# Performance work log

Hardware: AMD Instinct MI355X
Metric: run time of the kernel (lower is better)

Reference implementation:

```python
import jax, jax.numpy as jnp
from jax import lax
import numpy as np

IMG = 500
FM = 31
RATIOS = [1.0, 2.0, 0.5]
SCALES = [128, 256, 512]
PRE_NMS = 6000
POST_NMS = 1500  # train_nms_topn (test=False)
IOU_THR = 0.7
VARIANCES = np.array([0.1, 0.1, 0.2, 0.2], np.float32)
BATCH = 16


def _gen_anchors():
    # bbox_utils.generate_anchors: normalized [y1,x1,y2,x2], grid of 31x31 centers,
    # 9 base shapes from (scale, ratio), clipped to [0,1].
    ctr = (np.arange(FM, dtype=np.float32) + 0.5) / FM
    cy, cx = np.meshgrid(ctr, ctr, indexing='ij')          # [FM,FM]
    base = []
    for s in SCALES:
        for r in RATIOS:
            w = s * np.sqrt(r) / IMG
            h = s / np.sqrt(r) / IMG
            base.append([h, w])
    base = np.array(base, np.float32)                       # [9,2]
    h, w = base[:, 0], base[:, 1]
    cy = cy[..., None]; cx = cx[..., None]                  # [FM,FM,1]
    anc = np.stack([cy - h / 2, cx - w / 2, cy + h / 2, cx + w / 2], axis=-1)
    return np.clip(anc.reshape(-1, 4), 0.0, 1.0).astype(np.float32)  # [8649,4]


def setup_inputs() -> dict:
    key = jax.random.key(0)
    k1, k2 = jax.random.split(key)
    return {
        'rpn_bbox_deltas': jax.random.normal(k1, (BATCH, FM, FM, 36), jnp.float32),
        'rpn_probs': jax.random.uniform(k2, (BATCH, FM, FM, 9), jnp.float32),
        'anchors': jnp.asarray(_gen_anchors()),
    }


def _nms_keep(boxes, scores):
    # Greedy NMS over score-descending-sorted boxes; returns keep mask [N].
    N = boxes.shape[0]
    y1, x1, y2, x2 = boxes[:, 0], boxes[:, 1], boxes[:, 2], boxes[:, 3]
    area = (y2 - y1) * (x2 - x1)

    def body(i, state):
        supp, keep, cnt = state
        valid = jnp.logical_and(jnp.logical_not(supp[i]), cnt < POST_NMS)
        keep = keep.at[i].set(valid)
        cnt = cnt + valid.astype(jnp.int32)
        ih = jnp.maximum(jnp.minimum(y2[i], y2) - jnp.maximum(y1[i], y1), 0.0)
        iw = jnp.maximum(jnp.minimum(x2[i], x2) - jnp.maximum(x1[i], x1), 0.0)
        inter = ih * iw
        iou = inter / (area[i] + area - inter + 1e-8)
        supp = jnp.where(valid, jnp.logical_or(supp, iou > IOU_THR), supp)
        return supp, keep, cnt

    supp0 = jnp.zeros((N,), bool)
    keep0 = jnp.zeros((N,), bool)
    _, keep, _ = lax.fori_loop(0, N, body, (supp0, keep0, jnp.int32(0)))
    return keep


def reference(rpn_bbox_deltas, rpn_probs, anchors):
    B = rpn_bbox_deltas.shape[0]
    N = anchors.shape[0]
    deltas = rpn_bbox_deltas.reshape(B, N, 4) * jnp.asarray(VARIANCES)  # [B,N,4]
    probs = rpn_probs.reshape(B, N)                                     # [B,N]

    # decode anchor deltas -> boxes
    anc_h = anchors[:, 2] - anchors[:, 0]
    anc_w = anchors[:, 3] - anchors[:, 1]
    ctr_y = anchors[:, 0] + 0.5 * anc_h
    ctr_x = anchors[:, 1] + 0.5 * anc_w
    bh = jnp.exp(deltas[..., 2]) * anc_h
    bw = jnp.exp(deltas[..., 3]) * anc_w
    bcy = deltas[..., 0] * anc_h + ctr_y
    bcx = deltas[..., 1] * anc_w + ctr_x
    y1 = bcy - 0.5 * bh
    x1 = bcx - 0.5 * bw
    boxes = jnp.stack([y1, x1, y1 + bh, x1 + bw], axis=-1)              # [B,N,4]

    # pre-NMS top-k by objectness (sorted descending)
    top_scores, top_idx = lax.top_k(probs, PRE_NMS)                     # [B,PRE_NMS]
    top_boxes = jnp.take_along_axis(boxes, top_idx[..., None], axis=1)  # [B,PRE_NMS,4]

    # greedy NMS (selection is non-differentiable, compute on stopped values)
    keep = jax.vmap(_nms_keep)(lax.stop_gradient(top_boxes),
                               lax.stop_gradient(top_scores))           # [B,PRE_NMS] bool

    # compact kept entries to the front, zero-pad to POST_NMS (combined NMS semantics)
    rank = jnp.cumsum(keep, axis=1) - 1
    slot = jnp.where(keep, rank, POST_NMS)  # dropped entries go to overflow slot

    def _scatter(sl, bx, sc, k):
        ob = jnp.zeros((POST_NMS + 1, 4), bx.dtype).at[sl].set(jnp.where(k[:, None], bx, 0.0))
        os = jnp.zeros((POST_NMS + 1,), sc.dtype).at[sl].set(jnp.where(k, sc, 0.0))
        return ob[:POST_NMS], os[:POST_NMS]

    roi_bboxes, roi_scores = jax.vmap(_scatter)(slot, top_boxes, top_scores, keep)
    roi_bboxes = jnp.clip(roi_bboxes, 0.0, 1.0)  # clip_boxes=True in combined NMS
    return roi_bboxes, roi_scores
```

## Files before the change

### kernel.cpp

```cpp
#include <hip/hip_runtime.h>
#include <hip/hip_bf16.h>

#define BATCH   16
#define N_ANC   8649
#define SORT_N  16384
#define PRE     6000
#define POST    1500
#define ROWW    188
#define MROWS   6016
#define NGRP    188
#define TI      256
#define TJ      256

__global__ __launch_bounds__(256) void k_decode(
    const float* __restrict__ deltas, const float* __restrict__ probs,
    const float* __restrict__ anchors, float4* __restrict__ boxes,
    unsigned long long* __restrict__ keys)
{
    int t = blockIdx.x * 256 + threadIdx.x;
    if (t >= BATCH * SORT_N) return;
    int b = t / SORT_N;
    int n = t - b * SORT_N;
    if (n >= N_ANC) { keys[t] = ~0ULL; return; }

    float s = probs[(size_t)b * N_ANC + n];
    unsigned int bits = __float_as_uint(s);
    unsigned int u = bits ^ ((bits & 0x80000000u) ? 0xFFFFFFFFu : 0x80000000u);
    keys[(size_t)b * SORT_N + n] = ((unsigned long long)(~u) << 32) | (unsigned int)n;

    float4 a = ((const float4*)anchors)[n];
    float4 d = ((const float4*)deltas)[(size_t)b * N_ANC + n];
    float dy = d.x * 0.1f, dx = d.y * 0.1f, dh = d.z * 0.2f, dw = d.w * 0.2f;
    float ah = a.z - a.x, aw = a.w - a.y;
    float cy = a.x + 0.5f * ah, cx = a.y + 0.5f * aw;
    float bh = expf(dh) * ah, bw = expf(dw) * aw;
    float bcy = dy * ah + cy, bcx = dx * aw + cx;
    float y1 = bcy - 0.5f * bh, x1 = bcx - 0.5f * bw;
    boxes[(size_t)b * N_ANC + n] = make_float4(y1, x1, y1 + bh, x1 + bw);
}

__global__ __launch_bounds__(1024) void k_sort(unsigned long long* __restrict__ keys)
{
    __shared__ unsigned long long sb[8192];
    int b = blockIdx.x;
    unsigned long long* kb = keys + (size_t)b * SORT_N;

    for (int c = 0; c < 2; c++) {
        unsigned long long* g = kb + c * 8192;
        for (int t = threadIdx.x; t < 8192; t += 1024) sb[t] = g[t];
        __syncthreads();
        for (int k = 2; k <= 8192; k <<= 1) {
            for (int j = k >> 1; j >= 1; j >>= 1) {
                for (int p = threadIdx.x; p < 4096; p += 1024) {
                    int i  = ((p & ~(j - 1)) << 1) | (p & (j - 1));
                    int gi = (c << 13) | i;
                    bool asc = ((gi & k) == 0);
                    unsigned long long a = sb[i], b2 = sb[i | j];
                    bool sw = asc ? (a > b2) : (a < b2);
                    if (sw) { sb[i] = b2; sb[i | j] = a; }
                }
                __syncthreads();
            }
        }
        for (int t = threadIdx.x; t < 8192; t += 1024) g[t] = sb[t];
        __syncthreads();
    }

    for (int p = threadIdx.x; p < 8192; p += 1024) {
        unsigned long long a = kb[p], b2 = kb[p + 8192];
        if (a > b2) { kb[p] = b2; kb[p + 8192] = a; }
    }
    __syncthreads();

    for (int t = threadIdx.x; t < 8192; t += 1024) sb[t] = kb[t];
    __syncthreads();
    for (int j = 4096; j >= 1; j >>= 1) {
        for (int p = threadIdx.x; p < 4096; p += 1024) {
            int i = ((p & ~(j - 1)) << 1) | (p & (j - 1));
            unsigned long long a = sb[i], b2 = sb[i | j];
            if (a > b2) { sb[i] = b2; sb[i | j] = a; }
        }
        __syncthreads();
    }
    for (int t = threadIdx.x; t < 6016; t += 1024) kb[t] = sb[t];
}

__global__ __launch_bounds__(256) void k_gather(
    const unsigned long long* __restrict__ keys, const float4* __restrict__ boxes,
    const float* __restrict__ probs,
    float4* __restrict__ sboxes, float* __restrict__ sscores)
{
    int t = blockIdx.x * 256 + threadIdx.x;
    if (t >= BATCH * PRE) return;
    int b = t / PRE;
    int r = t - b * PRE;
    unsigned long long k = keys[(size_t)b * SORT_N + r];
    int idx = (int)(k & 0xFFFFFFFFu);
    sboxes[(size_t)b * PRE + r]  = boxes[(size_t)b * N_ANC + idx];
    sscores[(size_t)b * PRE + r] = probs[(size_t)b * N_ANC + idx];
}

__global__ __launch_bounds__(256) void k_iou(
    const float4* __restrict__ sboxes, unsigned int* __restrict__ mask,
    unsigned int* __restrict__ diag)
{
    int it = blockIdx.x;
    int jt = blockIdx.y;
    int b  = blockIdx.z;
    if (jt < it) return;

    __shared__ float4 jb[TJ];
    __shared__ float  ja[TJ];
    int t = threadIdx.x;
    int j = jt * TJ + t;
    float4 bj = (j < PRE) ? sboxes[(size_t)b * PRE + j]
                          : make_float4(-2e6f, -2e6f, -1.5e6f, -1.5e6f);
    jb[t] = bj;
    ja[t] = (bj.z - bj.x) * (bj.w - bj.y);
    __syncthreads();

    int i = it * TI + t;
    if (i >= PRE) return;
    float4 bi = sboxes[(size_t)b * PRE + i];
    float areai = (bi.z - bi.x) * (bi.w - bi.y);

    unsigned int w[8];
    if (jt > it) {
        for (int wq = 0; wq < 8; wq++) {
            unsigned int bits = 0u;
            #pragma unroll
            for (int jj = 0; jj < 32; jj++) {
                int lj = wq * 32 + jj;
                float4 bx = jb[lj];
                float ih = fmaxf(fminf(bi.z, bx.z) - fmaxf(bi.x, bx.x), 0.0f);
                float iw = fmaxf(fminf(bi.w, bx.w) - fmaxf(bi.y, bx.y), 0.0f);
                float inter = ih * iw;
                float iou = inter / (areai + ja[lj] - inter + 1e-8f);
                if (iou > 0.7f) bits |= (1u << jj);
            }
            w[wq] = bits;
        }
    } else {
        unsigned int dw = 0u;
        for (int wq = 0; wq < 8; wq++) {
            int jbase = jt * TJ + wq * 32;
            unsigned int bits = 0u;
            if (jbase + 31 > i) {
                #pragma unroll
                for (int jj = 0; jj < 32; jj++) {
                    int lj = wq * 32 + jj;
                    float4 bx = jb[lj];
                    float ih = fmaxf(fminf(bi.z, bx.z) - fmaxf(bi.x, bx.x), 0.0f);
                    float iw = fmaxf(fminf(bi.w, bx.w) - fmaxf(bi.y, bx.y), 0.0f);
                    float inter = ih * iw;
                    float iou = inter / (areai + ja[lj] - inter + 1e-8f);
                    if (iou > 0.7f && (jbase + jj) > i) bits |= (1u << jj);
                }
            }
            w[wq] = bits;
            if (wq == (t >> 5)) dw = bits;
        }
        diag[(size_t)b * MROWS + it * 256 + t] = dw;
    }

    unsigned int* row = mask + ((size_t)b * MROWS + i) * ROWW + jt * 8;
    ((uint4*)row)[0] = make_uint4(w[0], w[1], w[2], w[3]);
    if (jt < 23) ((uint4*)row)[1] = make_uint4(w[4], w[5], w[6], w[7]);
}

__global__ __launch_bounds__(64, 1) void k_scan(
    const unsigned int* __restrict__ mask, const unsigned int* __restrict__ diag,
    int* __restrict__ out_idx, int* __restrict__ out_cnt)
{
    int b = blockIdx.x;
    int lane = threadIdx.x;
    const unsigned int* mb = mask + (size_t)b * MROWS * ROWW;
    const unsigned int* db = diag + (size_t)b * MROWS;
    bool lact = (lane < 47);
    unsigned int lbit  = 1u << (lane & 31);
    unsigned int below = lbit - 1u;

    uint4 st = make_uint4(0, 0, 0, 0);
    int cnt = 0;
    int* oi = out_idx + b * POST;

    for (int g = 0; g < NGRP; g++) {
        const uint4* dt = (const uint4*)(db + g * 32);
        uint4 t0 = dt[0], t1 = dt[1], t2 = dt[2], t3 = dt[3];
        uint4 t4 = dt[4], t5 = dt[5], t6 = dt[6], t7 = dt[7];

        bool need = lact && (4 * lane + 3 >= g);
        const unsigned int* gp = mb + (size_t)g * 32 * ROWW + 4 * lane;
        uint4 r[32];
        #pragma unroll
        for (int k = 0; k < 32; k++)
            r[k] = need ? *(const uint4*)(gp + (size_t)k * ROWW)
                        : make_uint4(0, 0, 0, 0);

        unsigned int cword = (g & 2) ? ((g & 1) ? st.w : st.z)
                                     : ((g & 1) ? st.y : st.x);
        unsigned int swv = __shfl(cword, g >> 2);

        unsigned int tri[32];
        tri[0]=t0.x;  tri[1]=t0.y;  tri[2]=t0.z;  tri[3]=t0.w;
        tri[4]=t1.x;  tri[5]=t1.y;  tri[6]=t1.z;  tri[7]=t1.w;
        tri[8]=t2.x;  tri[9]=t2.y;  tri[10]=t2.z; tri[11]=t2.w;
        tri[12]=t3.x; tri[13]=t3.y; tri[14]=t3.z; tri[15]=t3.w;
        tri[16]=t4.x; tri[17]=t4.y; tri[18]=t4.z; tri[19]=t4.w;
        tri[20]=t5.x; tri[21]=t5.y; tri[22]=t5.z; tri[23]=t5.w;
        tri[24]=t6.x; tri[25]=t6.y; tri[26]=t6.z; tri[27]=t6.w;
        tri[28]=t7.x; tri[29]=t7.y; tri[30]=t7.z; tri[31]=t7.w;

        unsigned int valid = (g == NGRP - 1) ? 0xFFFFu : 0xFFFFFFFFu;
        unsigned int alive = ~swv & valid;
        unsigned int keepm = 0;
        #pragma unroll
        for (int k = 0; k < 32; k++) {
            unsigned int bit = (alive >> k) & 1u;
            keepm |= bit << k;
            alive &= ~((0u - bit) & tri[k]);
        }

        int need_n = POST - cnt;
        int rank = __popc(keepm & below);
        bool keep_me = (lane < 32) && (keepm & lbit) && (rank < need_n);
        unsigned long long bal = __ballot(keep_me);
        unsigned int keepm2 = (unsigned int)bal;
        if (keep_me) oi[cnt + rank] = g * 32 + lane;

        #pragma unroll
        for (int k = 0; k < 32; k++) {
            unsigned int m = 0u - ((keepm2 >> k) & 1u);
            st.x |= r[k].x & m; st.y |= r[k].y & m;
            st.z |= r[k].z & m; st.w |= r[k].w & m;
        }

        cnt += __popc(keepm2);
        if (cnt >= POST) break;
    }
    if (lane == 0) out_cnt[b] = cnt;
}

__global__ __launch_bounds__(256) void k_out(
    const float4* __restrict__ sboxes, const float* __restrict__ sscores,
    const int* __restrict__ out_idx, const int* __restrict__ out_cnt,
    float* __restrict__ out)
{
    int t = blockIdx.x * 256 + threadIdx.x;
    if (t >= BATCH * POST) return;
    int b = t / POST;
    int r = t - b * POST;
    float4 v = make_float4(0, 0, 0, 0);
    float sc = 0.f;
    if (r < out_cnt[b]) {
        int i = out_idx[b * POST + r];
        float4 bx = sboxes[(size_t)b * PRE + i];
        v.x = fminf(fmaxf(bx.x, 0.f), 1.f);
        v.y = fminf(fmaxf(bx.y, 0.f), 1.f);
        v.z = fminf(fmaxf(bx.z, 0.f), 1.f);
        v.w = fminf(fmaxf(bx.w, 0.f), 1.f);
        sc = sscores[(size_t)b * PRE + i];
    }
    ((float4*)out)[t] = v;
    out[(size_t)BATCH * POST * 4 + t] = sc;
}

extern "C" void kernel_launch(void* const* d_in, const int* in_sizes, int n_in,
                              void* d_out, int out_size, void* d_ws, size_t ws_size,
                              hipStream_t stream)
{
    const float* deltas  = (const float*)d_in[0];
    const float* probs   = (const float*)d_in[1];
    const float* anchors = (const float*)d_in[2];
    float* out = (float*)d_out;

    char* ws = (char*)d_ws;
    size_t off = 0;
    auto alloc = [&](size_t bytes) {
        size_t o = off;
        off = (off + bytes + 255) & ~(size_t)255;
        return o;
    };
    float4* boxes            = (float4*)(ws + alloc((size_t)BATCH * N_ANC * 16));
    unsigned long long* keys = (unsigned long long*)(ws + alloc((size_t)BATCH * SORT_N * 8));
    float4* sboxes           = (float4*)(ws + alloc((size_t)BATCH * PRE * 16));
    float* sscores           = (float*)(ws + alloc((size_t)BATCH * PRE * 4));
    unsigned int* mask       = (unsigned int*)(ws + alloc((size_t)BATCH * MROWS * ROWW * 4));
    unsigned int* diag       = (unsigned int*)(ws + alloc((size_t)BATCH * MROWS * 4));
    int* oidx                = (int*)(ws + alloc((size_t)BATCH * POST * 4));
    int* ocnt                = (int*)(ws + alloc((size_t)BATCH * 4));

    k_decode<<<(BATCH * SORT_N + 255) / 256, 256, 0, stream>>>(deltas, probs, anchors, boxes, keys);
    k_sort<<<BATCH, 1024, 0, stream>>>(keys);
    k_gather<<<(BATCH * PRE + 255) / 256, 256, 0, stream>>>(keys, boxes, probs, sboxes, sscores);
    k_iou<<<dim3(24, 24, BATCH), 256, 0, stream>>>(sboxes, mask, diag);
    k_scan<<<BATCH, 64, 0, stream>>>(mask, diag, oidx, ocnt);
    k_out<<<(BATCH * POST + 255) / 256, 256, 0, stream>>>(sboxes, sscores, oidx, ocnt, out);
}
```

Baseline: 710.8 us.

## Split IoU mask and scan into two phases to skip unneeded tiles

```diff
diff --git a/kernel.cpp b/kernel.cpp
--- a/kernel.cpp
+++ b/kernel.cpp
@@ -9,6 +9,7 @@
 #define ROWW    188
 #define MROWS   6016
 #define NGRP    188
+#define GLIM    64
 #define TI      256
 #define TJ      256
 
@@ -100,14 +101,16 @@
     sscores[(size_t)b * PRE + r] = probs[(size_t)b * N_ANC + idx];
 }
 
+template<int IT0, bool CHK>
 __global__ __launch_bounds__(256) void k_iou(
     const float4* __restrict__ sboxes, unsigned int* __restrict__ mask,
-    unsigned int* __restrict__ diag)
-{
-    int it = blockIdx.x;
+    unsigned int* __restrict__ diag, const int* __restrict__ done)
+{
+    int it = IT0 + blockIdx.x;
     int jt = blockIdx.y;
     int b  = blockIdx.z;
     if (jt < it) return;
+    if (CHK && done[b]) return;
 
     __shared__ float4 jb[TJ];
     __shared__ float  ja[TJ];
@@ -168,9 +171,10 @@
     if (jt < 23) ((uint4*)row)[1] = make_uint4(w[4], w[5], w[6], w[7]);
 }
 
-__global__ __launch_bounds__(64, 1) void k_scan(
+__global__ __launch_bounds__(64, 1) void k_scan_a(
     const unsigned int* __restrict__ mask, const unsigned int* __restrict__ diag,
-    int* __restrict__ out_idx, int* __restrict__ out_cnt)
+    int* __restrict__ out_idx, int* __restrict__ out_cnt,
+    uint4* __restrict__ stbuf, int* __restrict__ done)
 {
     int b = blockIdx.x;
     int lane = threadIdx.x;
@@ -184,7 +188,7 @@
     int cnt = 0;
     int* oi = out_idx + b * POST;
 
-    for (int g = 0; g < NGRP; g++) {
+    for (int g = 0; g < GLIM; g++) {
         const uint4* dt = (const uint4*)(db + g * 32);
         uint4 t0 = dt[0], t1 = dt[1], t2 = dt[2], t3 = dt[3];
         uint4 t4 = dt[4], t5 = dt[5], t6 = dt[6], t7 = dt[7];
@@ -211,8 +215,7 @@
         tri[24]=t6.x; tri[25]=t6.y; tri[26]=t6.z; tri[27]=t6.w;
         tri[28]=t7.x; tri[29]=t7.y; tri[30]=t7.z; tri[31]=t7.w;
 
-        unsigned int valid = (g == NGRP - 1) ? 0xFFFFu : 0xFFFFFFFFu;
-        unsigned int alive = ~swv & valid;
+        unsigned int alive = ~swv;
         unsigned int keepm = 0;
         #pragma unroll
         for (int k = 0; k < 32; k++) {
@@ -234,7 +237,81 @@
             st.x |= r[k].x & m; st.y |= r[k].y & m;
             st.z |= r[k].z & m; st.w |= r[k].w & m;
         }
-
+        cnt += __popc(keepm2);
+    }
+
+    if (lact) stbuf[b * 47 + lane] = st;
+    if (lane == 0) { out_cnt[b] = cnt; done[b] = (cnt >= POST) ? 1 : 0; }
+}
+
+__global__ __launch_bounds__(64, 1) void k_scan_b(
+    const unsigned int* __restrict__ mask, const unsigned int* __restrict__ diag,
+    int* __restrict__ out_idx, int* __restrict__ out_cnt,
+    const uint4* __restrict__ stbuf, const int* __restrict__ done)
+{
+    int b = blockIdx.x;
+    if (done[b]) return;
+    int lane = threadIdx.x;
+    const unsigned int* mb = mask + (size_t)b * MROWS * ROWW;
+    const unsigned int* db = diag + (size_t)b * MROWS;
+    bool lact = (lane < 47);
+    unsigned int lbit  = 1u << (lane & 31);
+    unsigned int below = lbit - 1u;
+
+    uint4 st = lact ? stbuf[b * 47 + lane] : make_uint4(0, 0, 0, 0);
+    int cnt = out_cnt[b];
+    int* oi = out_idx + b * POST;
+
+    for (int g = GLIM; g < NGRP; g++) {
+        const uint4* dt = (const uint4*)(db + g * 32);
+        uint4 t0 = dt[0], t1 = dt[1], t2 = dt[2], t3 = dt[3];
+        uint4 t4 = dt[4], t5 = dt[5], t6 = dt[6], t7 = dt[7];
+
+        bool need = lact && (4 * lane + 3 >= g);
+        const unsigned int* gp = mb + (size_t)g * 32 * ROWW + 4 * lane;
+        uint4 r[32];
+        #pragma unroll
+        for (int k = 0; k < 32; k++)
+            r[k] = need ? *(const uint4*)(gp + (size_t)k * ROWW)
+                        : make_uint4(0, 0, 0, 0);
+
+        unsigned int cword = (g & 2) ? ((g & 1) ? st.w : st.z)
+                                     : ((g & 1) ? st.y : st.x);
+        unsigned int swv = __shfl(cword, g >> 2);
+
+        unsigned int tri[32];
+        tri[0]=t0.x;  tri[1]=t0.y;  tri[2]=t0.z;  tri[3]=t0.w;
+        tri[4]=t1.x;  tri[5]=t1.y;  tri[6]=t1.z;  tri[7]=t1.w;
+        tri[8]=t2.x;  tri[9]=t2.y;  tri[10]=t2.z; tri[11]=t2.w;
+        tri[12]=t3.x; tri[13]=t3.y; tri[14]=t3.z; tri[15]=t3.w;
+        tri[16]=t4.x; tri[17]=t4.y; tri[18]=t4.z; tri[19]=t4.w;
+        tri[20]=t5.x; tri[21]=t5.y; tri[22]=t5.z; tri[23]=t5.w;
+        tri[24]=t6.x; tri[25]=t6.y; tri[26]=t6.z; tri[27]=t6.w;
+        tri[28]=t7.x; tri[29]=t7.y; tri[30]=t7.z; tri[31]=t7.w;
+
+        unsigned int valid = (g == NGRP - 1) ? 0xFFFFu : 0xFFFFFFFFu;
+        unsigned int alive = ~swv & valid;
+        unsigned int keepm = 0;
+        #pragma unroll
+        for (int k = 0; k < 32; k++) {
+            unsigned int bit = (alive >> k) & 1u;
+            keepm |= bit << k;
+            alive &= ~((0u - bit) & tri[k]);
+        }
+
+        int need_n = POST - cnt;
+        int rank = __popc(keepm & below);
+        bool keep_me = (lane < 32) && (keepm & lbit) && (rank < need_n);
+        unsigned long long bal = __ballot(keep_me);
+        unsigned int keepm2 = (unsigned int)bal;
+        if (keep_me) oi[cnt + rank] = g * 32 + lane;
+
+        #pragma unroll
+        for (int k = 0; k < 32; k++) {
+            unsigned int m = 0u - ((keepm2 >> k) & 1u);
+            st.x |= r[k].x & m; st.y |= r[k].y & m;
+            st.z |= r[k].z & m; st.w |= r[k].w & m;
+        }
         cnt += __popc(keepm2);
         if (cnt >= POST) break;
     }
@@ -289,11 +366,15 @@
     unsigned int* diag       = (unsigned int*)(ws + alloc((size_t)BATCH * MROWS * 4));
     int* oidx                = (int*)(ws + alloc((size_t)BATCH * POST * 4));
     int* ocnt                = (int*)(ws + alloc((size_t)BATCH * 4));
+    uint4* stbuf             = (uint4*)(ws + alloc((size_t)BATCH * 47 * 16));
+    int* done                = (int*)(ws + alloc((size_t)BATCH * 4));
 
     k_decode<<<(BATCH * SORT_N + 255) / 256, 256, 0, stream>>>(deltas, probs, anchors, boxes, keys);
     k_sort<<<BATCH, 1024, 0, stream>>>(keys);
     k_gather<<<(BATCH * PRE + 255) / 256, 256, 0, stream>>>(keys, boxes, probs, sboxes, sscores);
-    k_iou<<<dim3(24, 24, BATCH), 256, 0, stream>>>(sboxes, mask, diag);
-    k_scan<<<BATCH, 64, 0, stream>>>(mask, diag, oidx, ocnt);
+    k_iou<0, false><<<dim3(8, 24, BATCH), 256, 0, stream>>>(sboxes, mask, diag, done);
+    k_scan_a<<<BATCH, 64, 0, stream>>>(mask, diag, oidx, ocnt, stbuf, done);
+    k_iou<8, true><<<dim3(16, 24, BATCH), 256, 0, stream>>>(sboxes, mask, diag, done);
+    k_scan_b<<<BATCH, 64, 0, stream>>>(mask, diag, oidx, ocnt, stbuf, done);
     k_out<<<(BATCH * POST + 255) / 256, 256, 0, stream>>>(sboxes, sscores, oidx, ocnt, out);
 }
```

After: 779.2 us. 9.6% more time.

## Split sort across blocks, widen IoU tiles, double-buffer NMS scan loads

Applied to the files above, without the earlier changes.

```diff
diff --git a/kernel.cpp b/kernel.cpp
--- a/kernel.cpp
+++ b/kernel.cpp
@@ -6,11 +6,9 @@
 #define SORT_N  16384
 #define PRE     6000
 #define POST    1500
-#define ROWW    188
+#define RWORDS  192
 #define MROWS   6016
 #define NGRP    188
-#define TI      256
-#define TJ      256
 
 __global__ __launch_bounds__(256) void k_decode(
     const float* __restrict__ deltas, const float* __restrict__ probs,
@@ -39,32 +37,36 @@
     boxes[(size_t)b * N_ANC + n] = make_float4(y1, x1, y1 + bh, x1 + bw);
 }
 
-__global__ __launch_bounds__(1024) void k_sort(unsigned long long* __restrict__ keys)
+__global__ __launch_bounds__(1024) void k_sort_chunk(unsigned long long* __restrict__ keys)
+{
+    __shared__ unsigned long long sb[8192];
+    int b = blockIdx.x >> 1;
+    int c = blockIdx.x & 1;
+    unsigned long long* g = keys + (size_t)b * SORT_N + c * 8192;
+
+    for (int t = threadIdx.x; t < 8192; t += 1024) sb[t] = g[t];
+    __syncthreads();
+    for (int k = 2; k <= 8192; k <<= 1) {
+        for (int j = k >> 1; j >= 1; j >>= 1) {
+            for (int p = threadIdx.x; p < 4096; p += 1024) {
+                int i  = ((p & ~(j - 1)) << 1) | (p & (j - 1));
+                int gi = (c << 13) | i;
+                bool asc = ((gi & k) == 0);
+                unsigned long long a = sb[i], b2 = sb[i | j];
+                bool sw = asc ? (a > b2) : (a < b2);
+                if (sw) { sb[i] = b2; sb[i | j] = a; }
+            }
+            __syncthreads();
+        }
+    }
+    for (int t = threadIdx.x; t < 8192; t += 1024) g[t] = sb[t];
+}
+
+__global__ __launch_bounds__(1024) void k_sort_merge(unsigned long long* __restrict__ keys)
 {
     __shared__ unsigned long long sb[8192];
     int b = blockIdx.x;
     unsigned long long* kb = keys + (size_t)b * SORT_N;
-
-    for (int c = 0; c < 2; c++) {
-        unsigned long long* g = kb + c * 8192;
-        for (int t = threadIdx.x; t < 8192; t += 1024) sb[t] = g[t];
-        __syncthreads();
-        for (int k = 2; k <= 8192; k <<= 1) {
-            for (int j = k >> 1; j >= 1; j >>= 1) {
-                for (int p = threadIdx.x; p < 4096; p += 1024) {
-                    int i  = ((p & ~(j - 1)) << 1) | (p & (j - 1));
-                    int gi = (c << 13) | i;
-                    bool asc = ((gi & k) == 0);
-                    unsigned long long a = sb[i], b2 = sb[i | j];
-                    bool sw = asc ? (a > b2) : (a < b2);
-                    if (sw) { sb[i] = b2; sb[i | j] = a; }
-                }
-                __syncthreads();
-            }
-        }
-        for (int t = threadIdx.x; t < 8192; t += 1024) g[t] = sb[t];
-        __syncthreads();
-    }
 
     for (int p = threadIdx.x; p < 8192; p += 1024) {
         unsigned long long a = kb[p], b2 = kb[p + 8192];
@@ -107,66 +109,104 @@
     int it = blockIdx.x;
     int jt = blockIdx.y;
     int b  = blockIdx.z;
-    if (jt < it) return;
-
-    __shared__ float4 jb[TJ];
-    __shared__ float  ja[TJ];
+    int ibase = it * 1024;
+    int jbase0 = jt * 256;
+    if (jbase0 + 255 <= ibase) return;
+
+    __shared__ float4 jb[256];
+    __shared__ float  ja[256];
     int t = threadIdx.x;
-    int j = jt * TJ + t;
+    int j = jbase0 + t;
     float4 bj = (j < PRE) ? sboxes[(size_t)b * PRE + j]
                           : make_float4(-2e6f, -2e6f, -1.5e6f, -1.5e6f);
     jb[t] = bj;
     ja[t] = (bj.z - bj.x) * (bj.w - bj.y);
     __syncthreads();
 
-    int i = it * TI + t;
-    if (i >= PRE) return;
-    float4 bi = sboxes[(size_t)b * PRE + i];
-    float areai = (bi.z - bi.x) * (bi.w - bi.y);
-
-    unsigned int w[8];
-    if (jt > it) {
-        for (int wq = 0; wq < 8; wq++) {
-            unsigned int bits = 0u;
+    float4 bi[4];
+    float  ai[4];
+    int    ir[4];
+    #pragma unroll
+    for (int r = 0; r < 4; r++) {
+        ir[r] = ibase + t + 256 * r;
+        bi[r] = (ir[r] < PRE) ? sboxes[(size_t)b * PRE + ir[r]]
+                              : make_float4(0.f, 0.f, 0.f, 0.f);
+        ai[r] = (bi[r].z - bi[r].x) * (bi[r].w - bi[r].y);
+    }
+
+    unsigned int w[4][8];
+    for (int wq = 0; wq < 8; wq++) {
+        int jbase = jbase0 + wq * 32;
+        unsigned int bits0 = 0, bits1 = 0, bits2 = 0, bits3 = 0;
+        #pragma unroll
+        for (int jj = 0; jj < 32; jj++) {
+            int lj = wq * 32 + jj;
+            float4 bx = jb[lj];
+            float  aj = ja[lj];
+            int    jg = jbase + jj;
             #pragma unroll
-            for (int jj = 0; jj < 32; jj++) {
-                int lj = wq * 32 + jj;
-                float4 bx = jb[lj];
-                float ih = fmaxf(fminf(bi.z, bx.z) - fmaxf(bi.x, bx.x), 0.0f);
-                float iw = fmaxf(fminf(bi.w, bx.w) - fmaxf(bi.y, bx.y), 0.0f);
+            for (int r = 0; r < 4; r++) {
+                float ih = fmaxf(fminf(bi[r].z, bx.z) - fmaxf(bi[r].x, bx.x), 0.0f);
+                float iw = fmaxf(fminf(bi[r].w, bx.w) - fmaxf(bi[r].y, bx.y), 0.0f);
                 float inter = ih * iw;
-                float iou = inter / (areai + ja[lj] - inter + 1e-8f);
-                if (iou > 0.7f) bits |= (1u << jj);
+                float iou = inter / (ai[r] + aj - inter + 1e-8f);
+                bool set = (iou > 0.7f) && (jg > ir[r]);
+                unsigned int bit = set ? (1u << jj) : 0u;
+                if (r == 0) bits0 |= bit;
+                else if (r == 1) bits1 |= bit;
+                else if (r == 2) bits2 |= bit;
+                else bits3 |= bit;
             }
-            w[wq] = bits;
-        }
-    } else {
-        unsigned int dw = 0u;
-        for (int wq = 0; wq < 8; wq++) {
-            int jbase = jt * TJ + wq * 32;
-            unsigned int bits = 0u;
-            if (jbase + 31 > i) {
-                #pragma unroll
-                for (int jj = 0; jj < 32; jj++) {
-                    int lj = wq * 32 + jj;
-                    float4 bx = jb[lj];
-                    float ih = fmaxf(fminf(bi.z, bx.z) - fmaxf(bi.x, bx.x), 0.0f);
-                    float iw = fmaxf(fminf(bi.w, bx.w) - fmaxf(bi.y, bx.y), 0.0f);
-                    float inter = ih * iw;
-                    float iou = inter / (areai + ja[lj] - inter + 1e-8f);
-                    if (iou > 0.7f && (jbase + jj) > i) bits |= (1u << jj);
-                }
-            }
-            w[wq] = bits;
-            if (wq == (t >> 5)) dw = bits;
-        }
-        diag[(size_t)b * MROWS + it * 256 + t] = dw;
-    }
-
-    unsigned int* row = mask + ((size_t)b * MROWS + i) * ROWW + jt * 8;
-    ((uint4*)row)[0] = make_uint4(w[0], w[1], w[2], w[3]);
-    if (jt < 23) ((uint4*)row)[1] = make_uint4(w[4], w[5], w[6], w[7]);
-}
+        }
+        w[0][wq] = bits0; w[1][wq] = bits1; w[2][wq] = bits2; w[3][wq] = bits3;
+    }
+
+    #pragma unroll
+    for (int r = 0; r < 4; r++) {
+        if (ir[r] < PRE) {
+            unsigned int* row = mask + ((size_t)b * MROWS + ir[r]) * RWORDS + jt * 8;
+            ((uint4*)row)[0] = make_uint4(w[r][0], w[r][1], w[r][2], w[r][3]);
+            ((uint4*)row)[1] = make_uint4(w[r][4], w[r][5], w[r][6], w[r][7]);
+            if ((ir[r] >> 8) == jt)
+                diag[(size_t)b * MROWS + ir[r]] = w[r][(ir[r] >> 5) & 7];
+        }
+    }
+}
+
+#define PROCESS_GROUP(G, R, T)                                                   \
+    do {                                                                         \
+        unsigned int cw_ = ((G) & 2) ? (((G) & 1) ? st.w : st.z)                 \
+                                     : (((G) & 1) ? st.y : st.x);                \
+        unsigned int swv_ = __shfl(cw_, (G) >> 2);                               \
+        unsigned int tri_[32];                                                   \
+        _Pragma("unroll")                                                        \
+        for (int q_ = 0; q_ < 8; q_++) {                                         \
+            tri_[4*q_]   = T[q_].x; tri_[4*q_+1] = T[q_].y;                      \
+            tri_[4*q_+2] = T[q_].z; tri_[4*q_+3] = T[q_].w;                      \
+        }                                                                        \
+        unsigned int valid_ = ((G) == NGRP - 1) ? 0xFFFFu : 0xFFFFFFFFu;         \
+        unsigned int alive_ = ~swv_ & valid_;                                    \
+        unsigned int keepm_ = 0;                                                 \
+        _Pragma("unroll")                                                        \
+        for (int k_ = 0; k_ < 32; k_++) {                                        \
+            unsigned int bit_ = (alive_ >> k_) & 1u;                             \
+            keepm_ |= bit_ << k_;                                                \
+            alive_ &= ~((0u - bit_) & tri_[k_]);                                 \
+        }                                                                        \
+        int need_ = POST - cnt;                                                  \
+        int rank_ = __popc(keepm_ & below);                                      \
+        bool kme_ = (lane < 32) && (keepm_ & lbit) && (rank_ < need_);           \
+        unsigned long long bal_ = __ballot(kme_);                                \
+        unsigned int km2_ = (unsigned int)bal_;                                  \
+        if (kme_) oi[cnt + rank_] = (G) * 32 + lane;                             \
+        _Pragma("unroll")                                                        \
+        for (int k_ = 0; k_ < 32; k_++) {                                        \
+            unsigned int m_ = 0u - ((km2_ >> k_) & 1u);                          \
+            st.x |= R[k_].x & m_; st.y |= R[k_].y & m_;                          \
+            st.z |= R[k_].z & m_; st.w |= R[k_].w & m_;                          \
+        }                                                                        \
+        cnt += __popc(km2_);                                                     \
+    } while (0)
 
 __global__ __launch_bounds__(64, 1) void k_scan(
     const unsigned int* __restrict__ mask, const unsigned int* __restrict__ diag,
@@ -174,9 +214,8 @@
 {
     int b = blockIdx.x;
     int lane = threadIdx.x;
-    const unsigned int* mb = mask + (size_t)b * MROWS * ROWW;
+    const uint4* m4 = (const uint4*)(mask + (size_t)b * MROWS * RWORDS);
     const unsigned int* db = diag + (size_t)b * MROWS;
-    bool lact = (lane < 47);
     unsigned int lbit  = 1u << (lane & 31);
     unsigned int below = lbit - 1u;
 
@@ -184,59 +223,34 @@
     int cnt = 0;
     int* oi = out_idx + b * POST;
 
-    for (int g = 0; g < NGRP; g++) {
-        const uint4* dt = (const uint4*)(db + g * 32);
-        uint4 t0 = dt[0], t1 = dt[1], t2 = dt[2], t3 = dt[3];
-        uint4 t4 = dt[4], t5 = dt[5], t6 = dt[6], t7 = dt[7];
-
-        bool need = lact && (4 * lane + 3 >= g);
-        const unsigned int* gp = mb + (size_t)g * 32 * ROWW + 4 * lane;
-        uint4 r[32];
+    uint4 rA[32], rB[32];
+    uint4 tA[8],  tB[8];
+
+    #pragma unroll
+    for (int k = 0; k < 32; k++) rA[k] = m4[(size_t)k * 48 + lane];
+    #pragma unroll
+    for (int q = 0; q < 8; q++) tA[q] = ((const uint4*)db)[q];
+
+    for (int g = 0; g < NGRP; g += 2) {
         #pragma unroll
         for (int k = 0; k < 32; k++)
-            r[k] = need ? *(const uint4*)(gp + (size_t)k * ROWW)
-                        : make_uint4(0, 0, 0, 0);
-
-        unsigned int cword = (g & 2) ? ((g & 1) ? st.w : st.z)
-                                     : ((g & 1) ? st.y : st.x);
-        unsigned int swv = __shfl(cword, g >> 2);
-
-        unsigned int tri[32];
-        tri[0]=t0.x;  tri[1]=t0.y;  tri[2]=t0.z;  tri[3]=t0.w;
-        tri[4]=t1.x;  tri[5]=t1.y;  tri[6]=t1.z;  tri[7]=t1.w;
-        tri[8]=t2.x;  tri[9]=t2.y;  tri[10]=t2.z; tri[11]=t2.w;
-        tri[12]=t3.x; tri[13]=t3.y; tri[14]=t3.z; tri[15]=t3.w;
-        tri[16]=t4.x; tri[17]=t4.y; tri[18]=t4.z; tri[19]=t4.w;
-        tri[20]=t5.x; tri[21]=t5.y; tri[22]=t5.z; tri[23]=t5.w;
-        tri[24]=t6.x; tri[25]=t6.y; tri[26]=t6.z; tri[27]=t6.w;
-        tri[28]=t7.x; tri[29]=t7.y; tri[30]=t7.z; tri[31]=t7.w;
-
-        unsigned int valid = (g == NGRP - 1) ? 0xFFFFu : 0xFFFFFFFFu;
-        unsigned int alive = ~swv & valid;
-        unsigned int keepm = 0;
+            rB[k] = m4[(size_t)((g + 1) * 32 + k) * 48 + lane];
         #pragma unroll
-        for (int k = 0; k < 32; k++) {
-            unsigned int bit = (alive >> k) & 1u;
-            keepm |= bit << k;
-            alive &= ~((0u - bit) & tri[k]);
-        }
-
-        int need_n = POST - cnt;
-        int rank = __popc(keepm & below);
-        bool keep_me = (lane < 32) && (keepm & lbit) && (rank < need_n);
-        unsigned long long bal = __ballot(keep_me);
-        unsigned int keepm2 = (unsigned int)bal;
-        if (keep_me) oi[cnt + rank] = g * 32 + lane;
-
-        #pragma unroll
-        for (int k = 0; k < 32; k++) {
-            unsigned int m = 0u - ((keepm2 >> k) & 1u);
-            st.x |= r[k].x & m; st.y |= r[k].y & m;
-            st.z |= r[k].z & m; st.w |= r[k].w & m;
-        }
-
-        cnt += __popc(keepm2);
-        if (cnt >= POST) break;
+        for (int q = 0; q < 8; q++)
+            tB[q] = ((const uint4*)(db + (g + 1) * 32))[q];
+
+        PROCESS_GROUP(g, rA, tA);
+
+        if (g + 2 < NGRP) {
+            #pragma unroll
+            for (int k = 0; k < 32; k++)
+                rA[k] = m4[(size_t)((g + 2) * 32 + k) * 48 + lane];
+            #pragma unroll
+            for (int q = 0; q < 8; q++)
+                tA[q] = ((const uint4*)(db + (g + 2) * 32))[q];
+        }
+
+        PROCESS_GROUP(g + 1, rB, tB);
     }
     if (lane == 0) out_cnt[b] = cnt;
 }
@@ -285,15 +299,16 @@
     unsigned long long* keys = (unsigned long long*)(ws + alloc((size_t)BATCH * SORT_N * 8));
     float4* sboxes           = (float4*)(ws + alloc((size_t)BATCH * PRE * 16));
     float* sscores           = (float*)(ws + alloc((size_t)BATCH * PRE * 4));
-    unsigned int* mask       = (unsigned int*)(ws + alloc((size_t)BATCH * MROWS * ROWW * 4));
+    unsigned int* mask       = (unsigned int*)(ws + alloc((size_t)BATCH * MROWS * RWORDS * 4));
     unsigned int* diag       = (unsigned int*)(ws + alloc((size_t)BATCH * MROWS * 4));
     int* oidx                = (int*)(ws + alloc((size_t)BATCH * POST * 4));
     int* ocnt                = (int*)(ws + alloc((size_t)BATCH * 4));
 
     k_decode<<<(BATCH * SORT_N + 255) / 256, 256, 0, stream>>>(deltas, probs, anchors, boxes, keys);
-    k_sort<<<BATCH, 1024, 0, stream>>>(keys);
+    k_sort_chunk<<<BATCH * 2, 1024, 0, stream>>>(keys);
+    k_sort_merge<<<BATCH, 1024, 0, stream>>>(keys);
     k_gather<<<(BATCH * PRE + 255) / 256, 256, 0, stream>>>(keys, boxes, probs, sboxes, sscores);
-    k_iou<<<dim3(24, 24, BATCH), 256, 0, stream>>>(sboxes, mask, diag);
+    k_iou<<<dim3(6, 24, BATCH), 256, 0, stream>>>(sboxes, mask, diag);
     k_scan<<<BATCH, 64, 0, stream>>>(mask, diag, oidx, ocnt);
     k_out<<<(BATCH * POST + 255) / 256, 256, 0, stream>>>(sboxes, sscores, oidx, ocnt, out);
 }
```

After: 833.9 us. +17.3%, slower.
